# Optimization experiments

Measured on AMD Instinct MI355X. Metric: run time of the kernel, lower is better.

Reference implementation:

```python
import jax, jax.numpy as jnp
import numpy as np


def setup_inputs() -> dict:
    key = jax.random.key(0)
    k1, k2 = jax.random.split(key)
    N, C = 1_000_000, 80
    feats = jax.random.normal(k1, (N, C), dtype=jnp.float32)
    coords = jax.random.uniform(k2, (N, 4), dtype=jnp.float32)
    return {"feats": feats, "coords": coords, "B": 1, "D": 1, "H": 360, "W": 360}


def reference(feats, coords, B, D, H, W):
    N = feats.shape[0]
    C = feats.shape[1]
    # quantize coords exactly as the torch module does
    icoords = jnp.clip((coords * 12).astype(jnp.int32), 0, H - 1)  # [N,4]
    feats = jnp.clip(feats, 0.5, 0.5)  # faithful: all values become 0.5
    ranks = (icoords[:, 0] * (W * D * B)
             + icoords[:, 1] * (D * B)
             + icoords[:, 2] * B
             + icoords[:, 3])
    order = jnp.argsort(ranks)
    feats = feats[order]
    icoords = icoords[order]
    ranks = ranks[order]
    # segment boundaries over sorted ranks (QuickCumsum intervals)
    kept = jnp.concatenate([jnp.ones((1,), bool), ranks[1:] != ranks[:-1]])
    seg_ids = jnp.cumsum(kept.astype(jnp.int32)) - 1  # [N], segment id per row
    # per-segment sums == x_prefix[ends] - x_prefix[starts] + x[starts]
    seg_sums = jax.ops.segment_sum(feats, seg_ids, num_segments=N)  # [N,C]
    # flattened voxel index (note: uses W and H exactly as in the source)
    geom = (icoords[:, 0]
            + icoords[:, 1] * W
            + icoords[:, 2] * H
            + icoords[:, 3]).astype(jnp.int32)
    # geom value taken at each segment's FIRST row (interval start), like the
    # torch code's geom_feats[interval_starts]; dump slot N holds non-starts
    seg_geom = (jnp.zeros((N + 1,), jnp.int32)
                .at[jnp.where(kept, seg_ids, N)].set(geom))[:N]
    # unused segments carry zero sums and index 0 -> harmless add of zeros
    out = jnp.zeros((B * D * H * W, C), feats.dtype).at[seg_geom].add(seg_sums)
    return out.reshape(B, D, H, W, C)
```

## Files before the change

kernel.cpp:

```cpp
#include <hip/hip_runtime.h>

#define LDS_RANKS 4096
#define NPART 8
#define COUNT_BLOCKS 512
#define TOTAL_BLOCKS 2048
#define FIN_BLOCKS (LDS_RANKS / 64)


__global__ void __launch_bounds__(256) qcs_fused(
    const float4* __restrict__ coords4, int N,
    const int* __restrict__ pB, const int* __restrict__ pD,
    const int* __restrict__ pH, const int* __restrict__ pW,
    int* __restrict__ tabs, float* __restrict__ out, int out_size)
{
    __shared__ int s_cnt[LDS_RANKS];
    __shared__ int s_enc[LDS_RANKS];

    if (blockIdx.x < COUNT_BLOCKS) {
        for (int j = threadIdx.x; j < LDS_RANKS; j += blockDim.x) {
            s_cnt[j] = 0;
            s_enc[j] = 0;
        }
        __syncthreads();

        const int B = *pB, D = *pD, H = *pH, W = *pW;
        const int m0 = W * D * B, m1 = D * B, m2 = B;
        const int hi = H - 1;
        const int stride = COUNT_BLOCKS * blockDim.x;

        for (int i = blockIdx.x * blockDim.x + threadIdx.x; i < N; i += stride) {
            float4 c = coords4[i];
            int i0 = min(max((int)(c.x * 12.0f), 0), hi);
            int i1 = min(max((int)(c.y * 12.0f), 0), hi);
            int i2 = min(max((int)(c.z * 12.0f), 0), hi);
            int i3 = min(max((int)(c.w * 12.0f), 0), hi);
            int rank = i0 * m0 + i1 * m1 + i2 * m2 + i3;
            if (rank < LDS_RANKS) {
                atomicAdd(&s_cnt[rank], 1);
                atomicMax(&s_enc[rank], N - i);
            }
        }
        __syncthreads();

        int* cp = tabs + (blockIdx.x & (NPART - 1)) * LDS_RANKS;
        int* ep = cp + NPART * LDS_RANKS;
        for (int r = threadIdx.x; r < LDS_RANKS; r += blockDim.x) {
            int c = s_cnt[r];
            if (c > 0) {
                atomicAdd(&cp[r], c);
                atomicMax(&ep[r], s_enc[r]);
            }
        }
    } else {
        int zb = blockIdx.x - COUNT_BLOCKS;
        int nzb = gridDim.x - COUNT_BLOCKS;
        int tid = zb * blockDim.x + threadIdx.x;
        int stride = nzb * blockDim.x;
        float4 z = make_float4(0.f, 0.f, 0.f, 0.f);
        float4* out4 = reinterpret_cast<float4*>(out);
        int n4 = out_size >> 2;
        for (int i = tid; i < n4; i += stride) out4[i] = z;
        for (int i = (n4 << 2) + tid; i < out_size; i += stride) out[i] = 0.0f;
    }
}

__global__ void __launch_bounds__(256) qcs_finish(
    const float4* __restrict__ coords4, int N, int C,
    const int* __restrict__ pH, const int* __restrict__ pW,
    const int* __restrict__ tabs, float* __restrict__ out)
{
    __shared__ int l_tot[4][64];
    __shared__ int l_mx[4][64];
    __shared__ int l_geomC[64];
    __shared__ float l_val[64];
    __shared__ int l_na;

    int ls = threadIdx.x & 63;
    int q = threadIdx.x >> 6;
    int s = blockIdx.x * 64 + ls;

    const int* cp = tabs;
    const int* ep = tabs + NPART * LDS_RANKS;
    int t0 = cp[(2 * q) * LDS_RANKS + s] + cp[(2 * q + 1) * LDS_RANKS + s];
    int m0 = max(ep[(2 * q) * LDS_RANKS + s], ep[(2 * q + 1) * LDS_RANKS + s]);
    l_tot[q][ls] = t0;
    l_mx[q][ls] = m0;
    if (threadIdx.x == 0) l_na = 0;
    __syncthreads();

    if (q == 0) {
        int tot = l_tot[0][ls] + l_tot[1][ls] + l_tot[2][ls] + l_tot[3][ls];
        int mx = max(max(l_mx[0][ls], l_mx[1][ls]), max(l_mx[2][ls], l_mx[3][ls]));
        if (tot > 0) {
            const int H = *pH, W = *pW;
            const int hi = H - 1;
            int i = N - mx;
            float4 c = coords4[i];
            int i0 = min(max((int)(c.x * 12.0f), 0), hi);
            int i1 = min(max((int)(c.y * 12.0f), 0), hi);
            int i2 = min(max((int)(c.z * 12.0f), 0), hi);
            int i3 = min(max((int)(c.w * 12.0f), 0), hi);
            int geom = i0 + i1 * W + i2 * H + i3;
            int slot = atomicAdd(&l_na, 1);
            l_geomC[slot] = geom * C;
            l_val[slot] = 0.5f * (float)tot;
        }
    }
    __syncthreads();

    int na = l_na;
    if (na == 0) return;

    if (C <= (int)blockDim.x) {
        int ept = blockDim.x / C;
        int e0 = threadIdx.x / C;
        int ch = threadIdx.x - e0 * C;
        if (e0 < ept) {
            for (int e = e0; e < na; e += ept)
                atomicAdd(&out[l_geomC[e] + ch], l_val[e]);
        }
    } else {
        for (int e = 0; e < na; ++e) {
            float v = l_val[e];
            for (int k = threadIdx.x; k < C; k += blockDim.x)
                atomicAdd(&out[l_geomC[e] + k], v);
        }
    }
}

extern "C" void kernel_launch(void* const* d_in, const int* in_sizes, int n_in,
                              void* d_out, int out_size, void* d_ws, size_t ws_size,
                              hipStream_t stream) {
    const float4* coords4 = (const float4*)d_in[1];
    const int* pB = (const int*)d_in[2];
    const int* pD = (const int*)d_in[3];
    const int* pH = (const int*)d_in[4];
    const int* pW = (const int*)d_in[5];

    const int N = in_sizes[1] / 4;
    const int C = in_sizes[0] / N;

    int* tabs = (int*)d_ws;
    float* out = (float*)d_out;
    const size_t tab_bytes = (size_t)2 * NPART * LDS_RANKS * sizeof(int);

    hipMemsetAsync(d_ws, 0, tab_bytes, stream);

    qcs_fused<<<TOTAL_BLOCKS, 256, 0, stream>>>(coords4, N, pB, pD, pH, pW,
                                                tabs, out, out_size);

    qcs_finish<<<FIN_BLOCKS, 256, 0, stream>>>(coords4, N, C, pH, pW, tabs, out);
}
```

Baseline: 25.13 us.

## Replace global atomic partitions with per-block partial tables and drop memset

Each counting block now writes its full LDS histogram and max-index table to a private slice of workspace using vectorized int4 stores. This removes the global atomics and the hipMemsetAsync launch. The count stage shrinks from 512 to 128 blocks, and the finish kernel reduces across all 128 partials per rank. The cost is that each count block handles more input, and the finish kernel reads much more partial data (128x4096x2 ints).

```diff
diff --git a/kernel.cpp b/kernel.cpp
--- a/kernel.cpp
+++ b/kernel.cpp
@@ -1,8 +1,7 @@
 #include <hip/hip_runtime.h>
 
 #define LDS_RANKS 4096
-#define NPART 8
-#define COUNT_BLOCKS 512
+#define CB 128
 #define TOTAL_BLOCKS 2048
 #define FIN_BLOCKS (LDS_RANKS / 64)
 
@@ -11,12 +10,13 @@
     const float4* __restrict__ coords4, int N,
     const int* __restrict__ pB, const int* __restrict__ pD,
     const int* __restrict__ pH, const int* __restrict__ pW,
-    int* __restrict__ tabs, float* __restrict__ out, int out_size)
+    int* __restrict__ tabs_cnt, int* __restrict__ tabs_enc,
+    float* __restrict__ out, int out_size)
 {
     __shared__ int s_cnt[LDS_RANKS];
     __shared__ int s_enc[LDS_RANKS];
 
-    if (blockIdx.x < COUNT_BLOCKS) {
+    if (blockIdx.x < CB) {
         for (int j = threadIdx.x; j < LDS_RANKS; j += blockDim.x) {
             s_cnt[j] = 0;
             s_enc[j] = 0;
@@ -26,7 +26,7 @@
         const int B = *pB, D = *pD, H = *pH, W = *pW;
         const int m0 = W * D * B, m1 = D * B, m2 = B;
         const int hi = H - 1;
-        const int stride = COUNT_BLOCKS * blockDim.x;
+        const int stride = CB * blockDim.x;
 
         for (int i = blockIdx.x * blockDim.x + threadIdx.x; i < N; i += stride) {
             float4 c = coords4[i];
@@ -42,18 +42,17 @@
         }
         __syncthreads();
 
-        int* cp = tabs + (blockIdx.x & (NPART - 1)) * LDS_RANKS;
-        int* ep = cp + NPART * LDS_RANKS;
-        for (int r = threadIdx.x; r < LDS_RANKS; r += blockDim.x) {
-            int c = s_cnt[r];
-            if (c > 0) {
-                atomicAdd(&cp[r], c);
-                atomicMax(&ep[r], s_enc[r]);
-            }
+        int4* cp = reinterpret_cast<int4*>(tabs_cnt + blockIdx.x * LDS_RANKS);
+        int4* ep = reinterpret_cast<int4*>(tabs_enc + blockIdx.x * LDS_RANKS);
+        const int4* sc = reinterpret_cast<const int4*>(s_cnt);
+        const int4* se = reinterpret_cast<const int4*>(s_enc);
+        for (int j = threadIdx.x; j < LDS_RANKS / 4; j += blockDim.x) {
+            cp[j] = sc[j];
+            ep[j] = se[j];
         }
     } else {
-        int zb = blockIdx.x - COUNT_BLOCKS;
-        int nzb = gridDim.x - COUNT_BLOCKS;
+        int zb = blockIdx.x - CB;
+        int nzb = gridDim.x - CB;
         int tid = zb * blockDim.x + threadIdx.x;
         int stride = nzb * blockDim.x;
         float4 z = make_float4(0.f, 0.f, 0.f, 0.f);
@@ -67,7 +66,8 @@
 __global__ void __launch_bounds__(256) qcs_finish(
     const float4* __restrict__ coords4, int N, int C,
     const int* __restrict__ pH, const int* __restrict__ pW,
-    const int* __restrict__ tabs, float* __restrict__ out)
+    const int* __restrict__ tabs_cnt, const int* __restrict__ tabs_enc,
+    float* __restrict__ out)
 {
     __shared__ int l_tot[4][64];
     __shared__ int l_mx[4][64];
@@ -79,18 +79,20 @@
     int q = threadIdx.x >> 6;
     int s = blockIdx.x * 64 + ls;
 
-    const int* cp = tabs;
-    const int* ep = tabs + NPART * LDS_RANKS;
-    int t0 = cp[(2 * q) * LDS_RANKS + s] + cp[(2 * q + 1) * LDS_RANKS + s];
-    int m0 = max(ep[(2 * q) * LDS_RANKS + s], ep[(2 * q + 1) * LDS_RANKS + s]);
-    l_tot[q][ls] = t0;
-    l_mx[q][ls] = m0;
+    int tot = 0, mx = 0;
+#pragma unroll 8
+    for (int p = q; p < CB; p += 4) {
+        tot += tabs_cnt[p * LDS_RANKS + s];
+        mx = max(mx, tabs_enc[p * LDS_RANKS + s]);
+    }
+    l_tot[q][ls] = tot;
+    l_mx[q][ls] = mx;
     if (threadIdx.x == 0) l_na = 0;
     __syncthreads();
 
     if (q == 0) {
-        int tot = l_tot[0][ls] + l_tot[1][ls] + l_tot[2][ls] + l_tot[3][ls];
-        int mx = max(max(l_mx[0][ls], l_mx[1][ls]), max(l_mx[2][ls], l_mx[3][ls]));
+        tot = l_tot[0][ls] + l_tot[1][ls] + l_tot[2][ls] + l_tot[3][ls];
+        mx = max(max(l_mx[0][ls], l_mx[1][ls]), max(l_mx[2][ls], l_mx[3][ls]));
         if (tot > 0) {
             const int H = *pH, W = *pW;
             const int hi = H - 1;
@@ -140,14 +142,13 @@
     const int N = in_sizes[1] / 4;
     const int C = in_sizes[0] / N;
 
-    int* tabs = (int*)d_ws;
+    int* tabs_cnt = (int*)d_ws;
+    int* tabs_enc = tabs_cnt + CB * LDS_RANKS;
     float* out = (float*)d_out;
-    const size_t tab_bytes = (size_t)2 * NPART * LDS_RANKS * sizeof(int);
-
-    hipMemsetAsync(d_ws, 0, tab_bytes, stream);
 
     qcs_fused<<<TOTAL_BLOCKS, 256, 0, stream>>>(coords4, N, pB, pD, pH, pW,
-                                                tabs, out, out_size);
+                                                tabs_cnt, tabs_enc, out, out_size);
 
-    qcs_finish<<<FIN_BLOCKS, 256, 0, stream>>>(coords4, N, C, pH, pW, tabs, out);
+    qcs_finish<<<FIN_BLOCKS, 256, 0, stream>>>(coords4, N, C, pH, pW,
+                                               tabs_cnt, tabs_enc, out);
 }
```

After: 27.02 us. +7.5%, slower.

## Replace workspace memset with in-kernel zeroing and flag-based handoff

Applied to the files above, without the earlier changes.

Removes the separate hipMemsetAsync of the partition tables. The first NPART count blocks now zero their own partition table and publish a magic flag. Other blocks spin on that flag before merging their counts into the table, and the finish kernel resets the flags for the next call. This saves a launch and its overhead. In exchange it relies on the flag blocks being scheduled, which can deadlock if they are not resident, and it depends on the flags workspace starting out not equal to the magic value.

```diff
diff --git a/kernel.cpp b/kernel.cpp
--- a/kernel.cpp
+++ b/kernel.cpp
@@ -5,18 +5,34 @@
 #define COUNT_BLOCKS 512
 #define TOTAL_BLOCKS 2048
 #define FIN_BLOCKS (LDS_RANKS / 64)
+#define MAGIC64 0x9E3779B97F4A7C15ull
 
 
 __global__ void __launch_bounds__(256) qcs_fused(
     const float4* __restrict__ coords4, int N,
     const int* __restrict__ pB, const int* __restrict__ pD,
     const int* __restrict__ pH, const int* __restrict__ pW,
-    int* __restrict__ tabs, float* __restrict__ out, int out_size)
+    int* __restrict__ tabs, unsigned long long* __restrict__ flags,
+    float* __restrict__ out, int out_size)
 {
     __shared__ int s_cnt[LDS_RANKS];
     __shared__ int s_enc[LDS_RANKS];
 
     if (blockIdx.x < COUNT_BLOCKS) {
+        if (blockIdx.x < NPART) {
+            int* cp = tabs + blockIdx.x * LDS_RANKS;
+            int* ep = cp + NPART * LDS_RANKS;
+            float4 z = make_float4(0.f, 0.f, 0.f, 0.f);
+            for (int j = threadIdx.x; j < LDS_RANKS / 4; j += blockDim.x) {
+                reinterpret_cast<float4*>(cp)[j] = z;
+                reinterpret_cast<float4*>(ep)[j] = z;
+            }
+            __threadfence();
+            __syncthreads();
+            if (threadIdx.x == 0)
+                atomicExch(&flags[blockIdx.x], MAGIC64);
+        }
+
         for (int j = threadIdx.x; j < LDS_RANKS; j += blockDim.x) {
             s_cnt[j] = 0;
             s_enc[j] = 0;
@@ -42,7 +58,15 @@
         }
         __syncthreads();
 
-        int* cp = tabs + (blockIdx.x & (NPART - 1)) * LDS_RANKS;
+        int p = blockIdx.x & (NPART - 1);
+        if (blockIdx.x >= NPART) {
+            if (threadIdx.x == 0) {
+                while (__hip_atomic_load(&flags[p], __ATOMIC_ACQUIRE,
+                                         __HIP_MEMORY_SCOPE_AGENT) != MAGIC64) {}
+            }
+            __syncthreads();
+        }
+        int* cp = tabs + p * LDS_RANKS;
         int* ep = cp + NPART * LDS_RANKS;
         for (int r = threadIdx.x; r < LDS_RANKS; r += blockDim.x) {
             int c = s_cnt[r];
@@ -67,13 +91,17 @@
 __global__ void __launch_bounds__(256) qcs_finish(
     const float4* __restrict__ coords4, int N, int C,
     const int* __restrict__ pH, const int* __restrict__ pW,
-    const int* __restrict__ tabs, float* __restrict__ out)
+    const int* __restrict__ tabs, unsigned long long* __restrict__ flags,
+    float* __restrict__ out)
 {
     __shared__ int l_tot[4][64];
     __shared__ int l_mx[4][64];
     __shared__ int l_geomC[64];
     __shared__ float l_val[64];
     __shared__ int l_na;
+
+    if (blockIdx.x == 0 && threadIdx.x < NPART)
+        flags[threadIdx.x] = 0ull;
 
     int ls = threadIdx.x & 63;
     int q = threadIdx.x >> 6;
@@ -141,13 +169,13 @@
     const int C = in_sizes[0] / N;
 
     int* tabs = (int*)d_ws;
+    unsigned long long* flags =
+        (unsigned long long*)(tabs + 2 * NPART * LDS_RANKS);
     float* out = (float*)d_out;
-    const size_t tab_bytes = (size_t)2 * NPART * LDS_RANKS * sizeof(int);
-
-    hipMemsetAsync(d_ws, 0, tab_bytes, stream);
 
     qcs_fused<<<TOTAL_BLOCKS, 256, 0, stream>>>(coords4, N, pB, pD, pH, pW,
-                                                tabs, out, out_size);
+                                                tabs, flags, out, out_size);
 
-    qcs_finish<<<FIN_BLOCKS, 256, 0, stream>>>(coords4, N, C, pH, pW, tabs, out);
+    qcs_finish<<<FIN_BLOCKS, 256, 0, stream>>>(coords4, N, C, pH, pW,
+                                               tabs, flags, out);
 }
```

After: 22.97 us. 1.09x faster.
